# Kernel optimization log

Measured on AMD Instinct MI355X. Metric: run time of the kernel, lower is better.

The kernel has to match this reference:

```python
import jax, jax.numpy as jnp
import numpy as np

B, V, M, H = 256, 128, 256, 1024
TIMING_DIM = 10          # ceil(log2(max_timesteps=1024))
DECAY_ALPHA = 0.99
IN_DIM = (V + TIMING_DIM + 1 + 1) * M  # 35840


def setup_inputs() -> dict:
    key = jax.random.key(0)
    ks = jax.random.split(key, 12)
    x = jax.random.uniform(ks[0], (B, V), dtype=jnp.float32)
    memory = jax.random.uniform(ks[1], (B, M, V), dtype=jnp.float32)
    memory_timings = jax.random.randint(ks[2], (B, M), 0, 1000).astype(jnp.int64)
    memory_surprise = jax.random.uniform(ks[3], (B, M), dtype=jnp.float32)
    last_prediction = jax.random.uniform(ks[4], (B, V), dtype=jnp.float32)
    s1 = 1.0 / np.sqrt(IN_DIM)
    s2 = 1.0 / np.sqrt(H)
    W1 = jax.random.uniform(ks[5], (IN_DIM, H), dtype=jnp.float32, minval=-s1, maxval=s1)
    b1 = jnp.zeros((H,), jnp.float32)
    Wg = jax.random.uniform(ks[6], (IN_DIM, H), dtype=jnp.float32, minval=-s1, maxval=s1)
    bg = jnp.zeros((H,), jnp.float32)
    W2 = jax.random.uniform(ks[7], (H, V), dtype=jnp.float32, minval=-s2, maxval=s2)
    b2 = jnp.zeros((V,), jnp.float32)
    return {"x": x, "memory": memory, "memory_timings": memory_timings,
            "memory_surprise": memory_surprise, "last_prediction": last_prediction,
            "W1": W1, "b1": b1, "Wg": Wg, "bg": bg, "W2": W2, "b2": b2}


def _step(x, memory, memory_timings, memory_surprise, last_prediction):
    # surprise of incoming token under last prediction
    surprise = -jnp.log(jnp.sum(x * last_prediction, axis=1) + 1e-8)  # [B]
    # age + decay
    timings = memory_timings + 1
    surp = memory_surprise * DECAY_ALPHA
    # ring-buffer roll, write newest at slot 0
    mem = jnp.roll(memory, 1, axis=1).at[:, 0, :].set(x)
    timings = jnp.roll(timings, 1, axis=1).at[:, 0].set(0)
    surp = jnp.roll(surp, 1, axis=1).at[:, 0].set(surprise)
    # sort by age ascending, gather memory/surprise
    idx = jnp.argsort(timings, axis=1)                               # [B,M]
    sorted_timings = jnp.take_along_axis(timings, idx, axis=1)       # [B,M]
    sorted_memory = jnp.take_along_axis(mem, idx[..., None], axis=1)  # [B,M,V]
    sorted_surprise = jnp.take_along_axis(surp, idx, axis=1)          # [B,M]
    # binary encode timings
    powers = 2 ** jnp.arange(TIMING_DIM, dtype=sorted_timings.dtype)
    bits = ((sorted_timings[..., None] // powers) % 2).astype(jnp.float32)  # [B,M,T]
    norm_t = sorted_timings.astype(jnp.float32) / (
        jnp.max(sorted_timings, axis=1, keepdims=True).astype(jnp.float32) + 1.0)
    pred_input = jnp.concatenate(
        [sorted_memory.reshape(B, -1), bits.reshape(B, -1),
         norm_t.reshape(B, -1), sorted_surprise.reshape(B, -1)], axis=1)  # [B, IN_DIM]
    return pred_input


def reference(x, memory, memory_timings, memory_surprise, last_prediction,
              W1, b1, Wg, bg, W2, b2):
    pred_input = _step(x, memory, memory_timings, memory_surprise, last_prediction)
    # gated dense network: h = (xW1+b1) * sigmoid(xWg+bg); logits = hW2+b2
    h = (pred_input @ W1 + b1) * jax.nn.sigmoid(pred_input @ Wg + bg)
    return h @ W2 + b2
```

## Files before the change

### kernel.cpp

```cpp
#include <hip/hip_runtime.h>
#include <stdint.h>
#include <math.h>

#define BB 256
#define VV 128
#define MM 256
#define TDIM 10
#define HH 1024
#define IN_DIM 35840
#define KSPLIT 16
#define KSLICE 2240
#define BK 32
#define NCHUNK 70

using f32x4  = __attribute__((ext_vector_type(4))) float;
using bf16x8 = __attribute__((ext_vector_type(8))) short;

__device__ __forceinline__ unsigned short f2bf(float f) {
    unsigned int u = __float_as_uint(f);
    unsigned int r = (u + 0x7FFFu + ((u >> 16) & 1u)) >> 16;
    return (unsigned short)r;
}

__device__ __forceinline__ void gload_lds16(const void* g, void* l) {
    __builtin_amdgcn_global_load_lds(
        (const __attribute__((address_space(1))) unsigned int*)g,
        (__attribute__((address_space(3))) unsigned int*)l,
        16, 0, 0);
}

__global__ __launch_bounds__(256)
void k_build(const float* __restrict__ x, const float* __restrict__ memory,
             const int* __restrict__ timings, const float* __restrict__ msurp,
             const float* __restrict__ lastp, short* __restrict__ A)
{
    int b = blockIdx.x, t = threadIdx.x;
    __shared__ int t_s[MM], idx_s[MM], st_s[MM];
    __shared__ float red[MM];
    __shared__ float s_surprise;

    t_s[t] = (t == 0) ? 0 : timings[b*MM + t - 1] + 1;
    red[t] = (t < VV) ? x[b*VV + t] * lastp[b*VV + t] : 0.f;
    __syncthreads();
    for (int s = 128; s > 0; s >>= 1) {
        if (t < s) red[t] += red[t + s];
        __syncthreads();
    }
    if (t == 0) s_surprise = -logf(red[0] + 1e-8f);

    int ti = t_s[t], cnt = 0;
    #pragma unroll 4
    for (int j = 0; j < MM; ++j) {
        int tj = t_s[j];
        cnt += (tj < ti) || (tj == ti && j < t);
    }
    idx_s[cnt] = t;
    st_s[cnt]  = ti;
    __syncthreads();

    float invm = 1.f / ((float)st_s[MM-1] + 1.f);
    short* Ab = A + (size_t)b * IN_DIM;
    {
        int st = st_s[t], src = idx_s[t];
        #pragma unroll
        for (int tt = 0; tt < TDIM; ++tt)
            Ab[32768 + t*TDIM + tt] = (short)f2bf((float)((st >> tt) & 1));
        Ab[35328 + t] = (short)f2bf((float)st * invm);
        float sv = (src == 0) ? s_surprise : msurp[b*MM + src - 1] * 0.99f;
        Ab[35584 + t] = (short)f2bf(sv);
    }
    int half = t >> 7, v = t & (VV-1);
    for (int p = half; p < MM; p += 2) {
        int src = idx_s[p];
        float val = (src == 0) ? x[b*VV + v]
                               : memory[((size_t)b*MM + src - 1)*VV + v];
        Ab[p*VV + v] = (short)f2bf(val);
    }
}

__global__ __launch_bounds__(512, 4)
void k_gemm(const short* __restrict__ A, const float* __restrict__ W1,
            const float* __restrict__ Wg, float* __restrict__ P)
{
    int ks = blockIdx.x;
    int xt = blockIdx.y;
    const float* W = (xt < 16) ? W1 : Wg;
    int wcol0 = (xt & 15) * 64;
    int pcol0 = xt * 64;
    int k0 = ks * KSLICE;

    __shared__ bf16x8 As8[2][1024];
    __shared__ bf16x8 Ws8[2][256];

    int t = threadIdx.x;
    int l = t & 63, wv = t >> 6;
    int r = l & 15, q = l >> 4;
    int wm = wv & 3, nh = wv >> 2;

    int aoff[4], boff[2];
    #pragma unroll
    for (int mt = 0; mt < 4; ++mt) {
        int R = wm*64 + mt*16 + r;
        aoff[mt] = R*4 + (q ^ ((R >> 1) & 3));
    }
    #pragma unroll
    for (int nt = 0; nt < 2; ++nt) {
        int R = nh*32 + nt*16 + r;
        boff[nt] = R*4 + (q ^ ((R >> 1) & 3));
    }

    f32x4 acc[4][2];
    #pragma unroll
    for (int mt = 0; mt < 4; ++mt)
        #pragma unroll
        for (int nt = 0; nt < 2; ++nt)
            acc[mt][nt] = (f32x4){0.f, 0.f, 0.f, 0.f};

    int wn = l;
    int wkg = wv >> 1, whalf = wv & 1;
    int wslot16 = (wn*4 + (wkg ^ ((wn >> 1) & 3))) * 16 + whalf * 8;
    const float* wbase = W + (size_t)(k0 + wv*4)*HH + wcol0 + wn;
    float wreg[4];

    #pragma unroll
    for (int j = 0; j < 4; ++j) wreg[j] = wbase[(size_t)j*HH];
    {
        unsigned int lo = (unsigned int)f2bf(wreg[0]) | ((unsigned int)f2bf(wreg[1]) << 16);
        unsigned int hi = (unsigned int)f2bf(wreg[2]) | ((unsigned int)f2bf(wreg[3]) << 16);
        unsigned int* dst = (unsigned int*)((char*)&Ws8[0][0] + wslot16);
        dst[0] = lo; dst[1] = hi;
    }
    #pragma unroll
    for (int i = 0; i < 2; ++i) {
        int G = t + i*512;
        int m = G >> 2;
        int kb = (G & 3) ^ ((m >> 1) & 3);
        gload_lds16(A + (size_t)m*IN_DIM + k0 + kb*8,
                    (void*)(&As8[0][0] + (t & ~63) + i*512));
    }
    #pragma unroll
    for (int j = 0; j < 4; ++j) wreg[j] = wbase[(size_t)(BK*HH) + (size_t)j*HH];
    __syncthreads();

    for (int c = 0; c < NCHUNK; ++c) {
        int pb = c & 1, pn = pb ^ 1;
        {
            unsigned int lo = (unsigned int)f2bf(wreg[0]) | ((unsigned int)f2bf(wreg[1]) << 16);
            unsigned int hi = (unsigned int)f2bf(wreg[2]) | ((unsigned int)f2bf(wreg[3]) << 16);
            unsigned int* dst = (unsigned int*)((char*)&Ws8[pn][0] + wslot16);
            dst[0] = lo; dst[1] = hi;
        }
        {
            int cA = (c + 1 < NCHUNK) ? c + 1 : c;
            int kc = k0 + cA*BK;
            #pragma unroll
            for (int i = 0; i < 2; ++i) {
                int G = t + i*512;
                int m = G >> 2;
                int kb = (G & 3) ^ ((m >> 1) & 3);
                gload_lds16(A + (size_t)m*IN_DIM + kc + kb*8,
                            (void*)(&As8[pn][0] + (t & ~63) + i*512));
            }
        }
        {
            int cW = (c + 2 < NCHUNK) ? c + 2 : NCHUNK - 1;
            const float* wp = wbase + (size_t)cW*BK*HH;
            #pragma unroll
            for (int j = 0; j < 4; ++j) wreg[j] = wp[(size_t)j*HH];
        }
        {
            bf16x8 af[4], bfr[2];
            #pragma unroll
            for (int mt = 0; mt < 4; ++mt) af[mt] = As8[pb][aoff[mt]];
            #pragma unroll
            for (int nt = 0; nt < 2; ++nt) bfr[nt] = Ws8[pb][boff[nt]];
            #pragma unroll
            for (int mt = 0; mt < 4; ++mt)
                #pragma unroll
                for (int nt = 0; nt < 2; ++nt)
                    acc[mt][nt] = __builtin_amdgcn_mfma_f32_16x16x32_bf16(
                        af[mt], bfr[nt], acc[mt][nt], 0, 0, 0);
        }
        __syncthreads();
    }

    #pragma unroll
    for (int mt = 0; mt < 4; ++mt)
        #pragma unroll
        for (int nt = 0; nt < 2; ++nt)
            #pragma unroll
            for (int rg = 0; rg < 4; ++rg) {
                int m = wm*64 + mt*16 + q*4 + rg;
                int n = pcol0 + nh*32 + nt*16 + r;
                P[((size_t)ks*BB + m)*2048 + n] = acc[mt][nt][rg];
            }
}

__global__ __launch_bounds__(256)
void k_reduce(const float* __restrict__ P, const float* __restrict__ b1,
              const float* __restrict__ bg, float* __restrict__ h)
{
    int b = blockIdx.x, t = threadIdx.x;
    const f32x4* P4 = (const f32x4*)P;
    f32x4 p1 = ((const f32x4*)b1)[t];
    f32x4 pg = ((const f32x4*)bg)[t];
    #pragma unroll
    for (int ks = 0; ks < KSPLIT; ++ks) {
        size_t base = ((size_t)ks*BB + b) * 512;
        p1 += P4[base + t];
        pg += P4[base + 256 + t];
    }
    f32x4 o;
    #pragma unroll
    for (int j = 0; j < 4; ++j)
        o[j] = p1[j] / (1.f + expf(-pg[j]));
    ((f32x4*)h)[(size_t)b*256 + t] = o;
}

__global__ __launch_bounds__(256)
void k_out(const float* __restrict__ h, const float* __restrict__ W2,
           const float* __restrict__ b2, float* __restrict__ out)
{
    int b = blockIdx.x, t = threadIdx.x;
    int v = t & 127, kh = t >> 7;
    const float* hb = h + (size_t)b*HH + kh*512;
    const float* wp = W2 + (size_t)kh*512*VV + v;
    float acc = 0.f;
    #pragma unroll 8
    for (int k = 0; k < 512; ++k)
        acc += hb[k] * wp[(size_t)k*VV];
    __shared__ float s[256];
    s[t] = acc;
    __syncthreads();
    if (t < 128)
        out[(size_t)b*VV + v] = s[t] + s[t + 128] + b2[v];
}

extern "C" void kernel_launch(void* const* d_in, const int* in_sizes, int n_in,
                              void* d_out, int out_size, void* d_ws, size_t ws_size,
                              hipStream_t stream)
{
    const float* x    = (const float*)d_in[0];
    const float* mem  = (const float*)d_in[1];
    const int*   tim  = (const int*)d_in[2];
    const float* msur = (const float*)d_in[3];
    const float* lp   = (const float*)d_in[4];
    const float* W1   = (const float*)d_in[5];
    const float* b1   = (const float*)d_in[6];
    const float* Wg   = (const float*)d_in[7];
    const float* bg   = (const float*)d_in[8];
    const float* W2   = (const float*)d_in[9];
    const float* b2   = (const float*)d_in[10];
    float* out = (float*)d_out;

    short* A = (short*)d_ws;
    float* P = (float*)((char*)d_ws + 18350080);
    float* h = (float*)((char*)d_ws + 51904512);

    k_build <<<256, 256, 0, stream>>>(x, mem, tim, msur, lp, A);
    k_gemm  <<<dim3(KSPLIT, 32), 512, 0, stream>>>(A, W1, Wg, P);
    k_reduce<<<256, 256, 0, stream>>>(P, b1, bg, h);
    k_out   <<<256, 256, 0, stream>>>(h, W2, b2, out);
}
```

Baseline: 435.8 us.

## Triple-buffer GEMM with direct-to-LDS fp32 weight loads and deferred bf16 conversion

The GEMM mainloop now stages both the activation tile and the raw fp32 weight tile into LDS with asynchronous global_load_lds, using three buffers with vmcnt-based waits instead of register-staged weight conversion and double buffering. Weights are converted to bf16 per MFMA fragment when read from LDS, using an XOR swizzle on the column index. This removes register round-trips and gives a deeper prefetch for the memory-bound weight stream. In exchange it uses more LDS (fp32 weights, three stages), which may lower occupancy, and it adds scalar LDS reads plus conversion work in the inner loop.

```diff
diff --git a/kernel.cpp b/kernel.cpp
--- a/kernel.cpp
+++ b/kernel.cpp
@@ -89,24 +89,25 @@
     int pcol0 = xt * 64;
     int k0 = ks * KSLICE;
 
-    __shared__ bf16x8 As8[2][1024];
-    __shared__ bf16x8 Ws8[2][256];
+    __shared__ bf16x8 As8[3][1024];
+    __shared__ float  Wl[3][2048];
 
     int t = threadIdx.x;
     int l = t & 63, wv = t >> 6;
     int r = l & 15, q = l >> 4;
     int wm = wv & 3, nh = wv >> 2;
 
-    int aoff[4], boff[2];
+    int aoff[4];
     #pragma unroll
     for (int mt = 0; mt < 4; ++mt) {
         int R = wm*64 + mt*16 + r;
         aoff[mt] = R*4 + (q ^ ((R >> 1) & 3));
     }
+    int ncol[2];
     #pragma unroll
     for (int nt = 0; nt < 2; ++nt) {
-        int R = nh*32 + nt*16 + r;
-        boff[nt] = R*4 + (q ^ ((R >> 1) & 3));
+        int n = nh*32 + nt*16 + r;
+        ncol[nt] = n ^ (q << 4);
     }
 
     f32x4 acc[4][2];
@@ -116,73 +117,64 @@
         for (int nt = 0; nt < 2; ++nt)
             acc[mt][nt] = (f32x4){0.f, 0.f, 0.f, 0.f};
 
-    int wn = l;
-    int wkg = wv >> 1, whalf = wv & 1;
-    int wslot16 = (wn*4 + (wkg ^ ((wn >> 1) & 3))) * 16 + whalf * 8;
-    const float* wbase = W + (size_t)(k0 + wv*4)*HH + wcol0 + wn;
-    float wreg[4];
-
-    #pragma unroll
-    for (int j = 0; j < 4; ++j) wreg[j] = wbase[(size_t)j*HH];
-    {
-        unsigned int lo = (unsigned int)f2bf(wreg[0]) | ((unsigned int)f2bf(wreg[1]) << 16);
-        unsigned int hi = (unsigned int)f2bf(wreg[2]) | ((unsigned int)f2bf(wreg[3]) << 16);
-        unsigned int* dst = (unsigned int*)((char*)&Ws8[0][0] + wslot16);
-        dst[0] = lo; dst[1] = hi;
-    }
-    #pragma unroll
-    for (int i = 0; i < 2; ++i) {
-        int G = t + i*512;
-        int m = G >> 2;
-        int kb = (G & 3) ^ ((m >> 1) & 3);
-        gload_lds16(A + (size_t)m*IN_DIM + k0 + kb*8,
-                    (void*)(&As8[0][0] + (t & ~63) + i*512));
-    }
-    #pragma unroll
-    for (int j = 0; j < 4; ++j) wreg[j] = wbase[(size_t)(BK*HH) + (size_t)j*HH];
-    __syncthreads();
+    int wkk = t >> 4;
+    int wnF = ((t & 15) * 4) ^ (((wkk >> 3) & 3) << 4);
+
+#define STAGE(sbuf, cc) do {                                                  \
+        int kc_ = k0 + (cc)*BK;                                               \
+        {   int G_ = t;                                                       \
+            int m_ = G_ >> 2;                                                 \
+            int kb_ = (G_ & 3) ^ ((m_ >> 1) & 3);                             \
+            gload_lds16(A + (size_t)m_*IN_DIM + kc_ + kb_*8,                  \
+                        (char*)&As8[sbuf][0] + (size_t)(t & ~63)*16);         \
+        }                                                                     \
+        {   int G_ = t + 512;                                                 \
+            int m_ = G_ >> 2;                                                 \
+            int kb_ = (G_ & 3) ^ ((m_ >> 1) & 3);                             \
+            gload_lds16(A + (size_t)m_*IN_DIM + kc_ + kb_*8,                  \
+                        (char*)&As8[sbuf][0] + (size_t)((t & ~63) + 512)*16); \
+        }                                                                     \
+        gload_lds16(W + (size_t)(kc_ + wkk)*HH + wcol0 + wnF,                 \
+                    (char*)&Wl[sbuf][0] + (size_t)(t & ~63)*16);              \
+    } while (0)
+
+    STAGE(0, 0);
+    STAGE(1, 1);
+    STAGE(2, 2);
+    asm volatile("s_waitcnt vmcnt(6)" ::: "memory");
+    __builtin_amdgcn_s_barrier();
 
     for (int c = 0; c < NCHUNK; ++c) {
-        int pb = c & 1, pn = pb ^ 1;
+        int buf = c % 3;
+
+        bf16x8 af[4], bfr[2];
+        #pragma unroll
+        for (int mt = 0; mt < 4; ++mt) af[mt] = As8[buf][aoff[mt]];
+        #pragma unroll
+        for (int nt = 0; nt < 2; ++nt) {
+            const float* wb = &Wl[buf][ncol[nt]];
+            bf16x8 bb;
+            #pragma unroll
+            for (int j = 0; j < 8; ++j)
+                bb[j] = (short)f2bf(wb[(q*8 + j)*64]);
+            bfr[nt] = bb;
+        }
+        #pragma unroll
+        for (int mt = 0; mt < 4; ++mt)
+            #pragma unroll
+            for (int nt = 0; nt < 2; ++nt)
+                acc[mt][nt] = __builtin_amdgcn_mfma_f32_16x16x32_bf16(
+                    af[mt], bfr[nt], acc[mt][nt], 0, 0, 0);
+
+        __builtin_amdgcn_s_barrier();
         {
-            unsigned int lo = (unsigned int)f2bf(wreg[0]) | ((unsigned int)f2bf(wreg[1]) << 16);
-            unsigned int hi = (unsigned int)f2bf(wreg[2]) | ((unsigned int)f2bf(wreg[3]) << 16);
-            unsigned int* dst = (unsigned int*)((char*)&Ws8[pn][0] + wslot16);
-            dst[0] = lo; dst[1] = hi;
+            int cn = (c + 3 < NCHUNK) ? c + 3 : NCHUNK - 1;
+            STAGE(buf, cn);
         }
-        {
-            int cA = (c + 1 < NCHUNK) ? c + 1 : c;
-            int kc = k0 + cA*BK;
-            #pragma unroll
-            for (int i = 0; i < 2; ++i) {
-                int G = t + i*512;
-                int m = G >> 2;
-                int kb = (G & 3) ^ ((m >> 1) & 3);
-                gload_lds16(A + (size_t)m*IN_DIM + kc + kb*8,
-                            (void*)(&As8[pn][0] + (t & ~63) + i*512));
-            }
-        }
-        {
-            int cW = (c + 2 < NCHUNK) ? c + 2 : NCHUNK - 1;
-            const float* wp = wbase + (size_t)cW*BK*HH;
-            #pragma unroll
-            for (int j = 0; j < 4; ++j) wreg[j] = wp[(size_t)j*HH];
-        }
-        {
-            bf16x8 af[4], bfr[2];
-            #pragma unroll
-            for (int mt = 0; mt < 4; ++mt) af[mt] = As8[pb][aoff[mt]];
-            #pragma unroll
-            for (int nt = 0; nt < 2; ++nt) bfr[nt] = Ws8[pb][boff[nt]];
-            #pragma unroll
-            for (int mt = 0; mt < 4; ++mt)
-                #pragma unroll
-                for (int nt = 0; nt < 2; ++nt)
-                    acc[mt][nt] = __builtin_amdgcn_mfma_f32_16x16x32_bf16(
-                        af[mt], bfr[nt], acc[mt][nt], 0, 0, 0);
-        }
-        __syncthreads();
-    }
+        asm volatile("s_waitcnt vmcnt(6)" ::: "memory");
+        __builtin_amdgcn_s_barrier();
+    }
+#undef STAGE
 
     #pragma unroll
     for (int mt = 0; mt < 4; ++mt)
```

New measurement: 431.8 us. No clear change (-0.9%).
